# Kernel tuning notes

Measured on AMD Instinct MI355X. Metric: run time of the kernel, lower is better.

## Reference

```python
import jax, jax.numpy as jnp
import numpy as np

N_NODES = 100000
N_EDGES = 1600000


def _gcn_conv(h, W, b, src, dst, n):
    """PyG GCNConv: linear, add self-loops, sym-normalized scatter-add, bias."""
    h = h @ W  # [n, out]
    # degree with self-loops: 1 (self loop) + in-degree over dst
    deg = jnp.ones((n,), dtype=h.dtype).at[dst].add(1.0)
    dinv = jax.lax.rsqrt(deg)  # deg >= 1, safe
    norm = dinv[src] * dinv[dst]  # [E]
    out = jnp.zeros_like(h).at[dst].add(norm[:, None] * h[src])
    out = out + (dinv * dinv)[:, None] * h  # self-loop contribution
    return out + b


def setup_inputs() -> dict:
    key = jax.random.key(0)
    ks = jax.random.split(key, 6)
    x = jax.random.normal(ks[0], (N_NODES, 5), dtype=jnp.float32)
    edge_index = jax.random.randint(ks[1], (2, N_EDGES), 0, N_NODES, dtype=jnp.int64)
    aff_w = jax.random.normal(ks[2], (3, 1), dtype=jnp.float32)
    cog_w = jax.random.normal(ks[3], (2, 1), dtype=jnp.float32)
    W1 = jax.random.normal(ks[4], (5, 64), dtype=jnp.float32) * 0.5
    b1 = jnp.zeros((64,), dtype=jnp.float32)
    W2 = jax.random.normal(ks[5], (64, 2), dtype=jnp.float32) * 0.125
    b2 = jnp.zeros((2,), dtype=jnp.float32)
    return {"x": x, "edge_index": edge_index, "aff_w": aff_w, "cog_w": cog_w,
            "W1": W1, "b1": b1, "W2": W2, "b2": b2}


def reference(x, edge_index, aff_w, cog_w, W1, b1, W2, b2):
    src, dst = edge_index[0], edge_index[1]
    n = x.shape[0]
    aff = x[:, :3]  # affective_indices = [0,1,2]
    cog = x[:, 3:5]  # cognitive_indices = [3,4]
    # attention: scores are [n,1]; softmax over dim=1 (size-1 axis), faithful to source
    s_a = jax.nn.softmax(aff @ aff_w, axis=1)
    s_c = jax.nn.softmax(cog @ cog_w, axis=1)
    h = jnp.concatenate([aff * s_a, cog * s_c], axis=1)  # [n,5]
    h = _gcn_conv(h, W1, b1, src, dst, n)
    h = jax.nn.relu(h)  # dropout is identity in eval mode
    h = _gcn_conv(h, W2, b2, src, dst, n)
    return jax.nn.log_softmax(h, axis=1)
```

## Files before the change

kernel.cpp:

```cpp
#include <hip/hip_runtime.h>


#define NPB     256
#define BSHIFT  8
#define BINCAP  6144
#define MAXBINS 512
#define ABLK    512
#define APT     8
#define BBLK    512
#define ROUNDS  3

__global__ __launch_bounds__(ABLK) void binA_k(const int* __restrict__ src, const int* __restrict__ dst,
                                               int E, int nbins, int* __restrict__ cursor,
                                               unsigned int* __restrict__ bpk) {
    __shared__ int hist[MAXBINS];
    __shared__ int gbase[MAXBINS];
    int t = threadIdx.x;
    hist[t] = 0;
    __syncthreads();
    int base = blockIdx.x * (ABLK * APT);
    int s_[APT], d_[APT], r_[APT];
#pragma unroll
    for (int q = 0; q < APT; ++q) {
        int e = base + q * ABLK + t;
        if (e < E) {
            s_[q] = src[e]; d_[q] = dst[e];
            r_[q] = atomicAdd(&hist[d_[q] >> BSHIFT], 1);
        } else d_[q] = -1;
    }
    __syncthreads();
    if (t < nbins) {
        int h = hist[t];
        gbase[t] = h ? atomicAdd(&cursor[t], h) : 0;
    }
    __syncthreads();
#pragma unroll
    for (int q = 0; q < APT; ++q) {
        if (d_[q] >= 0) {
            int b = d_[q] >> BSHIFT;
            int pos = gbase[b] + r_[q];
            if (pos < BINCAP)
                bpk[(size_t)b * BINCAP + pos] = ((unsigned int)s_[q] << 8) | (unsigned int)(d_[q] & (NPB - 1));
        }
    }
}

__global__ __launch_bounds__(BBLK) void build_k(const int* __restrict__ cursor,
                                                const unsigned int* __restrict__ bpk,
                                                const float* __restrict__ x,
                                                int* __restrict__ sorted,
                                                int* __restrict__ row_start,
                                                unsigned short* __restrict__ row_cnt,
                                                float* __restrict__ dinv, float* __restrict__ y8, int n) {
    __shared__ int cnt[NPB];
    __shared__ int offs[NPB];
    __shared__ int srt[BINCAP];
    __shared__ int wsum[4];
    int b = blockIdx.x, t = threadIdx.x;
    if (t < NPB) cnt[t] = 0;
    __syncthreads();
    int m = cursor[b]; if (m > BINCAP) m = BINCAP;
    const unsigned int* pk = bpk + (size_t)b * BINCAP;

    unsigned int pv[ROUNDS][4];
    int rk[ROUNDS][4];
#pragma unroll
    for (int q = 0; q < ROUNDS; ++q) {
        int j0 = q * (BBLK * 4) + t * 4;
        if (j0 + 3 < m) {
            uint4 v = *(const uint4*)(pk + j0);
            pv[q][0] = v.x; pv[q][1] = v.y; pv[q][2] = v.z; pv[q][3] = v.w;
            rk[q][0] = atomicAdd(&cnt[v.x & 255u], 1);
            rk[q][1] = atomicAdd(&cnt[v.y & 255u], 1);
            rk[q][2] = atomicAdd(&cnt[v.z & 255u], 1);
            rk[q][3] = atomicAdd(&cnt[v.w & 255u], 1);
        } else {
#pragma unroll
            for (int qq = 0; qq < 4; ++qq) {
                int j = j0 + qq;
                if (j < m) { pv[q][qq] = pk[j]; rk[q][qq] = atomicAdd(&cnt[pv[q][qq] & 255u], 1); }
                else pv[q][qq] = 0xffffffffu;
            }
        }
    }
    __syncthreads();
    int c_ = 0, v = 0;
    int lane = t & 63, w = t >> 6;
    if (t < NPB) {
        c_ = cnt[t];
        v = c_;
#pragma unroll
        for (int dlt = 1; dlt < 64; dlt <<= 1) {
            int u = __shfl_up(v, dlt, 64);
            if (lane >= dlt) v += u;
        }
        if (lane == 63) wsum[w] = v;
    }
    __syncthreads();
    if (t < NPB) {
        int wo = 0;
#pragma unroll
        for (int k = 0; k < 4; ++k) if (k < w) wo += wsum[k];
        offs[t] = wo + v - c_;
    }
    __syncthreads();
#pragma unroll
    for (int q = 0; q < ROUNDS; ++q) {
#pragma unroll
        for (int qq = 0; qq < 4; ++qq) {
            unsigned int p = pv[q][qq];
            if (p != 0xffffffffu) {
                int j0 = q * (BBLK * 4) + t * 4 + qq;
                if (j0 < m) srt[offs[p & 255u] + rk[q][qq]] = (int)(p >> 8);
            }
        }
    }
    __syncthreads();
    int gb = b * BINCAP;
    for (int j0 = t * 4; j0 + 3 < m; j0 += BBLK * 4)
        *(int4*)(sorted + gb + j0) = *(const int4*)(srt + j0);
    if (t < 4) {
        int start = m & ~3;
        int j = start + t;
        if (j < m) sorted[gb + j] = srt[j];
    }
    int i = b * NPB + t;
    if (t < NPB && i < n) {
        row_start[i] = gb + offs[t];
        row_cnt[i] = (unsigned short)c_;
        float di = rsqrtf(1.0f + (float)c_);
        dinv[i] = di;
#pragma unroll
        for (int k = 0; k < 5; ++k) y8[(size_t)i * 8 + k] = di * x[i * 5 + k];
    }
}

__global__ __launch_bounds__(256) void gath1_mlp_k(const int* __restrict__ sorted,
                                                   const int* __restrict__ row_start,
                                                   const unsigned short* __restrict__ row_cnt,
                                                   const float* __restrict__ x, const float* __restrict__ y8,
                                                   const float* __restrict__ dinv,
                                                   const float* __restrict__ W1, const float* __restrict__ b1,
                                                   const float* __restrict__ W2,
                                                   float* __restrict__ g, float* __restrict__ gy, int n) {
    __shared__ float W1s[320], b1s[64], W2s[128];
    int t = threadIdx.x;
    { int j = t; if (j < 320) W1s[j] = W1[j]; j = t + 256; if (j < 320) W1s[j] = W1[j]; }
    if (t < 64) b1s[t] = b1[t];
    if (t >= 64 && t < 192) W2s[t - 64] = W2[t - 64];
    __syncthreads();
    int grp = t >> 2, lane = t & 3;
    int i = blockIdx.x * 64 + grp;
    if (i >= n) return;
    int st = row_start[i];
    int e  = st + row_cnt[i];
    float a0 = 0.f, a1 = 0.f, a2 = 0.f, a3 = 0.f, a4 = 0.f;
    for (int j = st + lane; j < e; j += 4) {
        int s = sorted[j];
        float4 A = *(const float4*)(y8 + (size_t)s * 8);
        a0 += A.x; a1 += A.y; a2 += A.z; a3 += A.w;
        a4 += y8[(size_t)s * 8 + 4];
    }
    a0 += __shfl_xor(a0, 1); a0 += __shfl_xor(a0, 2);
    a1 += __shfl_xor(a1, 1); a1 += __shfl_xor(a1, 2);
    a2 += __shfl_xor(a2, 1); a2 += __shfl_xor(a2, 2);
    a3 += __shfl_xor(a3, 1); a3 += __shfl_xor(a3, 2);
    a4 += __shfl_xor(a4, 1); a4 += __shfl_xor(a4, 2);
    float di = dinv[i], d2 = di * di;
    float v0 = di * a0 + d2 * x[i * 5 + 0];
    float v1 = di * a1 + d2 * x[i * 5 + 1];
    float v2 = di * a2 + d2 * x[i * 5 + 2];
    float v3 = di * a3 + d2 * x[i * 5 + 3];
    float v4 = di * a4 + d2 * x[i * 5 + 4];
    float g0 = 0.f, g1 = 0.f;
#pragma unroll
    for (int q = 0; q < 16; ++q) {
        int jj = lane + q * 4;
        float h = b1s[jj];
        h = fmaf(v0, W1s[0 * 64 + jj], h);
        h = fmaf(v1, W1s[1 * 64 + jj], h);
        h = fmaf(v2, W1s[2 * 64 + jj], h);
        h = fmaf(v3, W1s[3 * 64 + jj], h);
        h = fmaf(v4, W1s[4 * 64 + jj], h);
        h = fmaxf(h, 0.f);
        g0 = fmaf(h, W2s[2 * jj], g0);
        g1 = fmaf(h, W2s[2 * jj + 1], g1);
    }
    g0 += __shfl_xor(g0, 1); g0 += __shfl_xor(g0, 2);
    g1 += __shfl_xor(g1, 1); g1 += __shfl_xor(g1, 2);
    if (lane == 0) {
        g[i * 2] = g0;       g[i * 2 + 1] = g1;
        gy[i * 2] = di * g0; gy[i * 2 + 1] = di * g1;
    }
}

__global__ __launch_bounds__(256) void gath2_final_k(const int* __restrict__ sorted,
                                                     const int* __restrict__ row_start,
                                                     const unsigned short* __restrict__ row_cnt,
                                                     const float* __restrict__ g, const float* __restrict__ gy,
                                                     const float* __restrict__ dinv,
                                                     const float* __restrict__ b2,
                                                     float* __restrict__ out, int n) {
    int t = threadIdx.x;
    int grp = t >> 2, lane = t & 3;
    int i = blockIdx.x * 64 + grp;
    if (i >= n) return;
    int st = row_start[i];
    int e  = st + row_cnt[i];
    float t0 = 0.f, t1 = 0.f;
    for (int j = st + lane; j < e; j += 4) {
        int s = sorted[j];
        float2 v = *(const float2*)(gy + (size_t)s * 2);
        t0 += v.x; t1 += v.y;
    }
    t0 += __shfl_xor(t0, 1); t0 += __shfl_xor(t0, 2);
    t1 += __shfl_xor(t1, 1); t1 += __shfl_xor(t1, 2);
    if (lane == 0) {
        float di = dinv[i], d2 = di * di;
        float o0 = di * t0 + d2 * g[i * 2]     + b2[0];
        float o1 = di * t1 + d2 * g[i * 2 + 1] + b2[1];
        float mx = fmaxf(o0, o1);
        float lse = mx + logf(expf(o0 - mx) + expf(o1 - mx));
        out[i * 2]     = o0 - lse;
        out[i * 2 + 1] = o1 - lse;
    }
}

#define CAP 48
__global__ void fill_k(const int* __restrict__ src, const int* __restrict__ dst,
                       int E, int n, int* __restrict__ cnt, int* __restrict__ bucket) {
    int e = blockIdx.x * blockDim.x + threadIdx.x;
    if (e >= E) return;
    int s = src[e], d = dst[e];
    int slot = atomicAdd(&cnt[d], 1);
    if (slot < CAP) bucket[slot * n + d] = s;
}
__global__ void dinv_y_k(const float* __restrict__ x, const int* __restrict__ cnt,
                         float* __restrict__ dinv, float* __restrict__ y, int n) {
    int i = blockIdx.x * blockDim.x + threadIdx.x;
    if (i >= n) return;
    float di = rsqrtf(1.0f + (float)cnt[i]);
    dinv[i] = di;
#pragma unroll
    for (int k = 0; k < 5; ++k) y[i * 5 + k] = di * x[i * 5 + k];
}
__global__ void gather1_mlp_k(const float* __restrict__ x, const float* __restrict__ y,
                              const float* __restrict__ dinv, const int* __restrict__ cnt,
                              const int* __restrict__ bucket, int n,
                              const float* __restrict__ W1, const float* __restrict__ b1,
                              const float* __restrict__ W2,
                              float* __restrict__ g, float* __restrict__ gy) {
    __shared__ float W1s[320]; __shared__ float b1s[64]; __shared__ float W2s[128];
    int t = threadIdx.x;
    for (int j = t; j < 320; j += blockDim.x) W1s[j] = W1[j];
    if (t < 64) { b1s[t] = b1[t]; W2s[2 * t] = W2[2 * t]; W2s[2 * t + 1] = W2[2 * t + 1]; }
    __syncthreads();
    int i = blockIdx.x * blockDim.x + t;
    if (i >= n) return;
    int c = cnt[i]; if (c > CAP) c = CAP;
    float a0 = 0, a1 = 0, a2 = 0, a3 = 0, a4 = 0;
    for (int j = 0; j < c; ++j) {
        int s = bucket[j * n + i];
        const float* ys = y + s * 5;
        a0 += ys[0]; a1 += ys[1]; a2 += ys[2]; a3 += ys[3]; a4 += ys[4];
    }
    float di = dinv[i], d2 = di * di;
    float v0 = di * a0 + d2 * x[i * 5 + 0], v1 = di * a1 + d2 * x[i * 5 + 1];
    float v2 = di * a2 + d2 * x[i * 5 + 2], v3 = di * a3 + d2 * x[i * 5 + 3];
    float v4 = di * a4 + d2 * x[i * 5 + 4];
    float g0 = 0.f, g1 = 0.f;
#pragma unroll
    for (int j = 0; j < 64; ++j) {
        float h = b1s[j];
        h = fmaf(v0, W1s[j], h); h = fmaf(v1, W1s[64 + j], h); h = fmaf(v2, W1s[128 + j], h);
        h = fmaf(v3, W1s[192 + j], h); h = fmaf(v4, W1s[256 + j], h);
        h = fmaxf(h, 0.f);
        g0 = fmaf(h, W2s[2 * j], g0); g1 = fmaf(h, W2s[2 * j + 1], g1);
    }
    g[i * 2] = g0; g[i * 2 + 1] = g1;
    gy[i * 2] = di * g0; gy[i * 2 + 1] = di * g1;
}
__global__ void gather2_final_fb_k(const float* __restrict__ g, const float* __restrict__ gy,
                                   const float* __restrict__ dinv, const int* __restrict__ cnt,
                                   const int* __restrict__ bucket, int n,
                                   const float* __restrict__ b2, float* __restrict__ out) {
    int i = blockIdx.x * blockDim.x + threadIdx.x;
    if (i >= n) return;
    int c = cnt[i]; if (c > CAP) c = CAP;
    float t0 = 0.f, t1 = 0.f;
    for (int j = 0; j < c; ++j) {
        int s = bucket[j * n + i];
        t0 += gy[s * 2]; t1 += gy[s * 2 + 1];
    }
    float di = dinv[i], d2 = di * di;
    float o0 = di * t0 + d2 * g[i * 2] + b2[0];
    float o1 = di * t1 + d2 * g[i * 2 + 1] + b2[1];
    float mx = fmaxf(o0, o1);
    float lse = mx + logf(expf(o0 - mx) + expf(o1 - mx));
    out[i * 2] = o0 - lse; out[i * 2 + 1] = o1 - lse;
}

extern "C" void kernel_launch(void* const* d_in, const int* in_sizes, int n_in,
                              void* d_out, int out_size, void* d_ws, size_t ws_size,
                              hipStream_t stream) {
    const float* x  = (const float*)d_in[0];
    const int*   ei = (const int*)d_in[1];
    const float* W1 = (const float*)d_in[4];
    const float* b1 = (const float*)d_in[5];
    const float* W2 = (const float*)d_in[6];
    const float* b2 = (const float*)d_in[7];
    float* out = (float*)d_out;

    const int n = in_sizes[0] / 5;
    const int E = in_sizes[1] / 2;
    const int* src = ei;
    const int* dst = ei + E;

    const int nbins = (n + NPB - 1) >> BSHIFT;
    size_t need = (size_t)MAXBINS * 4 + (size_t)nbins * BINCAP * 8 +
                  (size_t)n * (4 + 2 + 4 + 32 + 8 + 8) + 64;

    if (nbins <= MAXBINS && n < (1 << 24) && ws_size >= need) {
        int* cursor = (int*)d_ws;
        unsigned int* bpk = (unsigned int*)(cursor + MAXBINS);
        int* sorted = (int*)(bpk + (size_t)nbins * BINCAP);
        int* row_start = sorted + (size_t)nbins * BINCAP;
        unsigned short* row_cnt = (unsigned short*)(row_start + n);
        float* dinv = (float*)(row_cnt + ((n + 1) & ~1));
        float* y8 = dinv + n;
        float* g  = y8 + 8 * (size_t)n;
        float* gy = g + 2 * (size_t)n;

        hipMemsetAsync(cursor, 0, MAXBINS * sizeof(int), stream);
        int ablocks = (E + ABLK * APT - 1) / (ABLK * APT);
        binA_k<<<ablocks, ABLK, 0, stream>>>(src, dst, E, nbins, cursor, bpk);
        build_k<<<nbins, BBLK, 0, stream>>>(cursor, bpk, x, sorted, row_start, row_cnt, dinv, y8, n);
        int g64 = (n + 63) / 64;
        gath1_mlp_k<<<g64, 256, 0, stream>>>(sorted, row_start, row_cnt, x, y8, dinv, W1, b1, W2, g, gy, n);
        gath2_final_k<<<g64, 256, 0, stream>>>(sorted, row_start, row_cnt, g, gy, dinv, b2, out, n);
    } else {
        const int BLK = 256;
        const int ngrid = (n + BLK - 1) / BLK;
        const int egrid = (E + BLK - 1) / BLK;
        int*   cnt    = (int*)d_ws;
        int*   bucket = cnt + n;
        float* dinv   = (float*)(bucket + (size_t)CAP * n);
        float* y      = dinv + n;
        float* g      = y + 5 * (size_t)n;
        float* gy     = g + 2 * (size_t)n;
        hipMemsetAsync(cnt, 0, (size_t)n * sizeof(int), stream);
        fill_k<<<egrid, BLK, 0, stream>>>(src, dst, E, n, cnt, bucket);
        dinv_y_k<<<ngrid, BLK, 0, stream>>>(x, cnt, dinv, y, n);
        gather1_mlp_k<<<ngrid, BLK, 0, stream>>>(x, y, dinv, cnt, bucket, n, W1, b1, W2, g, gy);
        gather2_final_fb_k<<<ngrid, BLK, 0, stream>>>(g, gy, dinv, cnt, bucket, n, b2, out);
    }
}
```

Before: 68.32 us.

## Replace rank-tracking with second atomic pass and scatter sorted edges directly to global

```diff
diff --git a/kernel.cpp b/kernel.cpp
--- a/kernel.cpp
+++ b/kernel.cpp
@@ -14,31 +14,31 @@
                                                int E, int nbins, int* __restrict__ cursor,
                                                unsigned int* __restrict__ bpk) {
     __shared__ int hist[MAXBINS];
-    __shared__ int gbase[MAXBINS];
     int t = threadIdx.x;
     hist[t] = 0;
     __syncthreads();
     int base = blockIdx.x * (ABLK * APT);
-    int s_[APT], d_[APT], r_[APT];
+    int s_[APT], d_[APT];
 #pragma unroll
     for (int q = 0; q < APT; ++q) {
         int e = base + q * ABLK + t;
         if (e < E) {
             s_[q] = src[e]; d_[q] = dst[e];
-            r_[q] = atomicAdd(&hist[d_[q] >> BSHIFT], 1);
+            atomicAdd(&hist[d_[q] >> BSHIFT], 1);
         } else d_[q] = -1;
     }
     __syncthreads();
     if (t < nbins) {
         int h = hist[t];
-        gbase[t] = h ? atomicAdd(&cursor[t], h) : 0;
+        int gb = h ? atomicAdd(&cursor[t], h) : 0;
+        hist[t] = gb;
     }
     __syncthreads();
 #pragma unroll
     for (int q = 0; q < APT; ++q) {
         if (d_[q] >= 0) {
             int b = d_[q] >> BSHIFT;
-            int pos = gbase[b] + r_[q];
+            int pos = atomicAdd(&hist[b], 1);
             if (pos < BINCAP)
                 bpk[(size_t)b * BINCAP + pos] = ((unsigned int)s_[q] << 8) | (unsigned int)(d_[q] & (NPB - 1));
         }
@@ -53,8 +53,6 @@
                                                 unsigned short* __restrict__ row_cnt,
                                                 float* __restrict__ dinv, float* __restrict__ y8, int n) {
     __shared__ int cnt[NPB];
-    __shared__ int offs[NPB];
-    __shared__ int srt[BINCAP];
     __shared__ int wsum[4];
     int b = blockIdx.x, t = threadIdx.x;
     if (t < NPB) cnt[t] = 0;
@@ -63,27 +61,27 @@
     const unsigned int* pk = bpk + (size_t)b * BINCAP;
 
     unsigned int pv[ROUNDS][4];
-    int rk[ROUNDS][4];
 #pragma unroll
     for (int q = 0; q < ROUNDS; ++q) {
         int j0 = q * (BBLK * 4) + t * 4;
         if (j0 + 3 < m) {
             uint4 v = *(const uint4*)(pk + j0);
             pv[q][0] = v.x; pv[q][1] = v.y; pv[q][2] = v.z; pv[q][3] = v.w;
-            rk[q][0] = atomicAdd(&cnt[v.x & 255u], 1);
-            rk[q][1] = atomicAdd(&cnt[v.y & 255u], 1);
-            rk[q][2] = atomicAdd(&cnt[v.z & 255u], 1);
-            rk[q][3] = atomicAdd(&cnt[v.w & 255u], 1);
+            atomicAdd(&cnt[v.x & 255u], 1);
+            atomicAdd(&cnt[v.y & 255u], 1);
+            atomicAdd(&cnt[v.z & 255u], 1);
+            atomicAdd(&cnt[v.w & 255u], 1);
         } else {
 #pragma unroll
             for (int qq = 0; qq < 4; ++qq) {
                 int j = j0 + qq;
-                if (j < m) { pv[q][qq] = pk[j]; rk[q][qq] = atomicAdd(&cnt[pv[q][qq] & 255u], 1); }
+                if (j < m) { pv[q][qq] = pk[j]; atomicAdd(&cnt[pv[q][qq] & 255u], 1); }
                 else pv[q][qq] = 0xffffffffu;
             }
         }
     }
     __syncthreads();
+    int gb = b * BINCAP;
     int c_ = 0, v = 0;
     int lane = t & 63, w = t >> 6;
     if (t < NPB) {
@@ -101,7 +99,17 @@
         int wo = 0;
 #pragma unroll
         for (int k = 0; k < 4; ++k) if (k < w) wo += wsum[k];
-        offs[t] = wo + v - c_;
+        int offs = wo + v - c_;
+        cnt[t] = offs;
+        int i = b * NPB + t;
+        if (i < n) {
+            row_start[i] = gb + offs;
+            row_cnt[i] = (unsigned short)c_;
+            float di = rsqrtf(1.0f + (float)c_);
+            dinv[i] = di;
+#pragma unroll
+            for (int k = 0; k < 5; ++k) y8[(size_t)i * 8 + k] = di * x[i * 5 + k];
+        }
     }
     __syncthreads();
 #pragma unroll
@@ -110,28 +118,10 @@
         for (int qq = 0; qq < 4; ++qq) {
             unsigned int p = pv[q][qq];
             if (p != 0xffffffffu) {
-                int j0 = q * (BBLK * 4) + t * 4 + qq;
-                if (j0 < m) srt[offs[p & 255u] + rk[q][qq]] = (int)(p >> 8);
+                int pos = atomicAdd(&cnt[p & 255u], 1);
+                sorted[gb + pos] = (int)(p >> 8);
             }
         }
-    }
-    __syncthreads();
-    int gb = b * BINCAP;
-    for (int j0 = t * 4; j0 + 3 < m; j0 += BBLK * 4)
-        *(int4*)(sorted + gb + j0) = *(const int4*)(srt + j0);
-    if (t < 4) {
-        int start = m & ~3;
-        int j = start + t;
-        if (j < m) sorted[gb + j] = srt[j];
-    }
-    int i = b * NPB + t;
-    if (t < NPB && i < n) {
-        row_start[i] = gb + offs[t];
-        row_cnt[i] = (unsigned short)c_;
-        float di = rsqrtf(1.0f + (float)c_);
-        dinv[i] = di;
-#pragma unroll
-        for (int k = 0; k < 5; ++k) y8[(size_t)i * 8 + k] = di * x[i * 5 + k];
     }
 }
 
```

After: 74.15 us. 1.09x slower.
